# Optimization experiments

Hardware: AMD Instinct MI355X
Metric: run time of the kernel (lower is better)

## Reference

```python
import jax, jax.numpy as jnp
import numpy as np

NUM_SEQ, NUM_RES = 512, 768
MSA_C, PAIR_C, NUM_HEAD = 64, 128, 8
VALUE_DIM = MSA_C // NUM_HEAD
EPS = 1e-5


def _layernorm(x, scale, bias):
    mu = jnp.mean(x, axis=-1, keepdims=True)
    var = jnp.var(x, axis=-1, keepdims=True)
    return (x - mu) * jax.lax.rsqrt(var + EPS) * scale + bias


def setup_inputs() -> dict:
    key = jax.random.key(0)
    ks = jax.random.split(key, 8)
    act = jax.random.normal(ks[0], (NUM_SEQ, NUM_RES, MSA_C), dtype=jnp.float32)
    mask = jnp.ones((NUM_SEQ, NUM_RES), dtype=jnp.float32)
    pair_act = jax.random.normal(ks[1], (NUM_RES, NUM_RES, PAIR_C), dtype=jnp.float32)
    # learned params
    act_scale = jnp.ones((MSA_C,), jnp.float32)
    act_bias = jnp.zeros((MSA_C,), jnp.float32)
    pair_scale = jnp.ones((PAIR_C,), jnp.float32)
    pair_bias = jnp.zeros((PAIR_C,), jnp.float32)
    w_pair_logits = jax.random.normal(ks[2], (NUM_HEAD, PAIR_C), jnp.float32) * (PAIR_C ** -0.5)
    v_proj = jax.random.normal(ks[3], (MSA_C, NUM_HEAD, VALUE_DIM), jnp.float32) * (MSA_C ** -0.5)
    w_gate = jax.random.normal(ks[4], (MSA_C, MSA_C), jnp.float32) * (MSA_C ** -0.5)
    w_out = jax.random.normal(ks[5], (MSA_C, MSA_C), jnp.float32) * (MSA_C ** -0.5)
    return {
        "act": act, "mask": mask, "pair_act": pair_act,
        "act_scale": act_scale, "act_bias": act_bias,
        "pair_scale": pair_scale, "pair_bias": pair_bias,
        "w_pair_logits": w_pair_logits, "v_proj": v_proj,
        "w_gate": w_gate, "w_out": w_out,
    }


def reference(act, mask, pair_act, act_scale, act_bias, pair_scale, pair_bias,
              w_pair_logits, v_proj, w_gate, w_out):
    act = _layernorm(act, act_scale, act_bias)            # [b, k, i]
    pair = _layernorm(pair_act, pair_scale, pair_bias)    # [q, k, c]
    logits = jnp.einsum('qkc,hc->hqk', pair, w_pair_logits)  # [h, q, k]
    # mask reduced over MSA rows; torch casts to bf16 before the bias add
    mask_max = jnp.max(mask, axis=0).astype(jnp.bfloat16)    # [k]
    logits = logits + 1e9 * (mask_max.astype(logits.dtype) - 1.0)
    weights = jax.nn.softmax(logits, axis=-1)                # [h, q, k]
    v = jnp.einsum('bki,ihc->bkhc', act, v_proj)             # [b, k, h, c]
    v_avg = jnp.einsum('hqk,bkhc->bqhc', weights, v)         # [b, q, h, c]
    v_avg = v_avg.reshape(v_avg.shape[0], v_avg.shape[1], -1)  # [b, q, h*c]
    gate = jax.nn.sigmoid(act @ w_gate.T)
    return (v_avg * gate) @ w_out.T
```

## Files before the change

kernel.cpp:

```cpp
#include <hip/hip_runtime.h>
#include <hip/hip_bf16.h>

#define NSEQ 512
#define NRES 768
#define MSAC 64
#define PAIRC 128
#define NHEAD 8

typedef __attribute__((ext_vector_type(8))) short short8_t;
typedef __attribute__((ext_vector_type(4))) float f32x4;

__device__ __forceinline__ float bf2f(unsigned short u){
  return __uint_as_float(((unsigned int)u) << 16);
}
__device__ __forceinline__ unsigned short f2bf(float f){
  unsigned int x = __float_as_uint(f);
  x += 0x7fffu + ((x >> 16) & 1u);
  return (unsigned short)(x >> 16);
}
__device__ __forceinline__ void glds16(const void* g, void* l){
  __builtin_amdgcn_global_load_lds(
      (const __attribute__((address_space(1))) unsigned int*)g,
      (__attribute__((address_space(3))) unsigned int*)l, 16, 0, 0);
}

__global__ __launch_bounds__(256) void k_prep2(
    const float* __restrict__ mask, const float* __restrict__ vproj,
    const float* __restrict__ wgate, const float* __restrict__ wout,
    const float* __restrict__ pscale, const float* __restrict__ pbias,
    const float* __restrict__ wl,
    float* __restrict__ bias, unsigned short* __restrict__ WvT,
    unsigned short* __restrict__ WgT, unsigned short* __restrict__ WoH,
    unsigned short* __restrict__ WoL, unsigned short* __restrict__ WST,
    float* __restrict__ AB)
{
  const int bid = blockIdx.x, tid = threadIdx.x;
  if (bid < 12){
    __shared__ float red[4][64];
    const int kk = bid*64 + (tid & 63);
    const int bs = tid >> 6;
    float m = -1e30f;
    for (int b = bs; b < NSEQ; b += 4) m = fmaxf(m, mask[(size_t)b*NRES + kk]);
    red[bs][tid & 63] = m;
    __syncthreads();
    if (tid < 64){
      float mm = fmaxf(fmaxf(red[0][tid], red[1][tid]),
                       fmaxf(red[2][tid], red[3][tid]));
      bias[bid*64 + tid] = 1e9f * (bf2f(f2bf(mm)) - 1.0f);
    }
  } else if (bid < 28){
    const int t = (bid - 12)*256 + tid;
    const int j = t >> 6, i = t & 63;
    WvT[t] = f2bf(vproj[i*64 + j]);
    WgT[t] = f2bf(wgate[t]);
    float wv = wout[t];
    unsigned short hh = f2bf(wv);
    WoH[t] = hh;
    WoL[t] = f2bf(wv - bf2f(hh));
  } else {
    #pragma unroll
    for (int i = 0; i < 4; ++i){
      int t = i*256 + tid;
      int h = t >> 7, c = t & 127;
      float w = pscale[c] * wl[h*PAIRC + c];
      unsigned short hh = f2bf(w);
      WST[h*PAIRC + c] = hh;
      WST[(h + 8)*PAIRC + c] = f2bf(w - bf2f(hh));
    }
    const int h = tid >> 5, cc = tid & 31;
    float pa = 0.f, pb = 0.f;
    for (int c = cc; c < PAIRC; c += 32){
      float w = wl[h*PAIRC + c];
      pa += pscale[c]*w;  pb += pbias[c]*w;
    }
    #pragma unroll
    for (int m = 1; m < 32; m <<= 1){
      pa += __shfl_xor(pa, m, 64);
      pb += __shfl_xor(pb, m, 64);
    }
    if (cc == 0){ AB[h] = pa; AB[8 + h] = pb; }
  }
}

__global__ __launch_bounds__(256) void k_pair(
    const float* __restrict__ pair, const unsigned short* __restrict__ WST,
    const float* __restrict__ AB, const float* __restrict__ mbias,
    unsigned short* __restrict__ weights)
{
  __shared__ float lg[NHEAD][NRES];
  const int q = blockIdx.x;
  const int tid = threadIdx.x;
  const int wv = tid >> 6, lane = tid & 63;
  const int lr = lane & 15, lcq = lane >> 4;

  short8_t wfrag[4];
  #pragma unroll
  for (int s = 0; s < 4; ++s)
    wfrag[s] = *(const short8_t*)(WST + lr*PAIRC + lcq*8 + s*32);

  const int hb = (lcq & 1) * 4;
  float A4[4], B4[4];
  #pragma unroll
  for (int r = 0; r < 4; ++r){ A4[r] = AB[hb + r]; B4[r] = AB[8 + hb + r]; }

  for (int tile = wv; tile < 48; tile += 4){
    const int k0 = tile * 16;
    const float* base = pair + ((size_t)q*NRES + k0 + lr)*PAIRC + lcq*8;
    f32x4 a1 = 0.f, a2 = 0.f;
    float s = 0.f, ss = 0.f;
    #pragma unroll
    for (int st = 0; st < 4; ++st){
      float4 u0 = *(const float4*)(base + st*32);
      float4 u1 = *(const float4*)(base + st*32 + 4);
      float xv[8] = {u0.x,u0.y,u0.z,u0.w,u1.x,u1.y,u1.z,u1.w};
      short8_t xh, xl;
      #pragma unroll
      for (int e = 0; e < 8; ++e){
        s += xv[e]; ss += xv[e]*xv[e];
        unsigned short hi = f2bf(xv[e]);
        xh[e] = (short)hi;
        xl[e] = (short)f2bf(xv[e] - bf2f(hi));
      }
      a1 = __builtin_amdgcn_mfma_f32_16x16x32_bf16(wfrag[st], xh, a1, 0, 0, 0);
      a2 = __builtin_amdgcn_mfma_f32_16x16x32_bf16(wfrag[st], xl, a2, 0, 0, 0);
    }
    s  += __shfl_xor(s, 16, 64);  ss += __shfl_xor(ss, 16, 64);
    s  += __shfl_xor(s, 32, 64);  ss += __shfl_xor(ss, 32, 64);
    const float mu  = s * (1.f/128.f);
    const float var = ss * (1.f/128.f) - mu*mu;
    const float rsq = rsqrtf(var + 1e-5f);
    float d[4];
    #pragma unroll
    for (int r = 0; r < 4; ++r)
      d[r] = a1[r] + __shfl_xor(a1[r], 32, 64) + a2[r];
    if (lane < 32){
      const int k = k0 + lr;
      #pragma unroll
      for (int r = 0; r < 4; ++r)
        lg[hb + r][k] = rsq * (d[r] - mu * A4[r]) + B4[r];
    }
  }
  __syncthreads();
  #pragma unroll
  for (int hh = 0; hh < 2; ++hh){
    int h = wv + hh*4;
    float mx = -1e30f;
    for (int kk = lane; kk < NRES; kk += 64) mx = fmaxf(mx, lg[h][kk] + mbias[kk]);
    #pragma unroll
    for (int m = 1; m < 64; m <<= 1) mx = fmaxf(mx, __shfl_xor(mx, m, 64));
    float sum = 0.f;
    for (int kk = lane; kk < NRES; kk += 64){
      float e = __expf(lg[h][kk] + mbias[kk] - mx);
      lg[h][kk] = e; sum += e;
    }
    #pragma unroll
    for (int m = 1; m < 64; m <<= 1) sum += __shfl_xor(sum, m, 64);
    float inv = 1.0f / sum;
    unsigned short* wrow = weights + ((size_t)h * NRES + q) * NRES;
    for (int kk = lane; kk < NRES; kk += 64) wrow[kk] = f2bf(lg[h][kk] * inv);
  }
}

__global__ __launch_bounds__(512) void k_act(
    const float* __restrict__ act, const float* __restrict__ ascale,
    const float* __restrict__ abias, const unsigned short* __restrict__ WvT,
    const unsigned short* __restrict__ WgT, unsigned short* __restrict__ v,
    unsigned short* __restrict__ gate)
{
  __shared__ __align__(16) unsigned char sm[18432];
  unsigned short (*vt)[72] = (unsigned short (*)[72])sm;
  unsigned short (*gt)[72] = (unsigned short (*)[72])(sm + 9216);
  const int abid = blockIdx.x;
  const int b  = abid / 6;
  const int k0 = (abid % 6) * 128;
  const int tid = threadIdx.x;
  const int w = tid >> 6, lane = tid & 63;
  const int lr = lane & 15;
  const int lc = lane >> 4;
  const int row = k0 + w*16 + lr;

  short8_t bv[4][2], bg[4][2];
  #pragma unroll
  for (int mf = 0; mf < 4; ++mf){
    #pragma unroll
    for (int s = 0; s < 2; ++s){
      bv[mf][s] = *(const short8_t*)(WvT + (mf*16 + lr)*64 + s*32 + lc*8);
      bg[mf][s] = *(const short8_t*)(WgT + (mf*16 + lr)*64 + s*32 + lc*8);
    }
  }

  const float* arow = act + ((size_t)b*NRES + row)*MSAC;
  float x[2][8];
  #pragma unroll
  for (int s = 0; s < 2; ++s){
    float4 t0 = *(const float4*)(arow + s*32 + lc*8);
    float4 t1 = *(const float4*)(arow + s*32 + lc*8 + 4);
    x[s][0]=t0.x; x[s][1]=t0.y; x[s][2]=t0.z; x[s][3]=t0.w;
    x[s][4]=t1.x; x[s][5]=t1.y; x[s][6]=t1.z; x[s][7]=t1.w;
  }
  float ps = 0.f, pss = 0.f;
  #pragma unroll
  for (int s = 0; s < 2; ++s)
    #pragma unroll
    for (int e = 0; e < 8; ++e){ ps += x[s][e]; pss += x[s][e]*x[s][e]; }
  ps  += __shfl_xor(ps, 16, 64);  pss += __shfl_xor(pss, 16, 64);
  ps  += __shfl_xor(ps, 32, 64);  pss += __shfl_xor(pss, 32, 64);
  const float mu  = ps * (1.f/64.f);
  const float var = pss * (1.f/64.f) - mu*mu;
  const float rs  = rsqrtf(var + 1e-5f);

  short8_t a[2];
  #pragma unroll
  for (int s = 0; s < 2; ++s){
    float4 s0 = *(const float4*)(ascale + s*32 + lc*8);
    float4 s1 = *(const float4*)(ascale + s*32 + lc*8 + 4);
    float4 b0 = *(const float4*)(abias  + s*32 + lc*8);
    float4 b1 = *(const float4*)(abias  + s*32 + lc*8 + 4);
    const float sc[8] = {s0.x,s0.y,s0.z,s0.w,s1.x,s1.y,s1.z,s1.w};
    const float bs[8] = {b0.x,b0.y,b0.z,b0.w,b1.x,b1.y,b1.z,b1.w};
    #pragma unroll
    for (int e = 0; e < 8; ++e)
      a[s][e] = (short)f2bf((x[s][e] - mu)*rs*sc[e] + bs[e]);
  }

  f32x4 accv[4], accg[4];
  #pragma unroll
  for (int mf = 0; mf < 4; ++mf){ accv[mf] = 0.f; accg[mf] = 0.f; }
  #pragma unroll
  for (int mf = 0; mf < 4; ++mf){
    #pragma unroll
    for (int s = 0; s < 2; ++s){
      accv[mf] = __builtin_amdgcn_mfma_f32_16x16x32_bf16(a[s], bv[mf][s], accv[mf], 0, 0, 0);
      accg[mf] = __builtin_amdgcn_mfma_f32_16x16x32_bf16(bg[mf][s], a[s], accg[mf], 0, 0, 0);
    }
  }

  #pragma unroll
  for (int pass = 0; pass < 2; ++pass){
    if ((w >> 2) == pass){
      const int wl2 = w & 3;
      #pragma unroll
      for (int mf = 0; mf < 4; ++mf){
        ushort4 ov;
        ov.x = f2bf(accv[mf][0]); ov.y = f2bf(accv[mf][1]);
        ov.z = f2bf(accv[mf][2]); ov.w = f2bf(accv[mf][3]);
        *(ushort4*)&vt[mf*16 + lr][wl2*16 + lc*4] = ov;
        ushort4 og;
        og.x = f2bf(1.0f/(1.0f + __expf(-accg[mf][0])));
        og.y = f2bf(1.0f/(1.0f + __expf(-accg[mf][1])));
        og.z = f2bf(1.0f/(1.0f + __expf(-accg[mf][2])));
        og.w = f2bf(1.0f/(1.0f + __expf(-accg[mf][3])));
        *(ushort4*)&gt[wl2*16 + lr][mf*16 + lc*4] = og;
      }
    }
    __syncthreads();
    {
      const int kbase = k0 + pass*64;
      const int j = tid >> 3, chunk = tid & 7;
      uint4 val = *(const uint4*)&vt[j][chunk*8];
      *(uint4*)(v + ((size_t)(j >> 3)*4096 + (size_t)b*8 + (j & 7))*NRES + kbase + chunk*8) = val;
      uint4 gval = *(const uint4*)&gt[j][chunk*8];
      *(uint4*)(gate + ((size_t)b*NRES + kbase + j)*MSAC + chunk*8) = gval;
    }
    __syncthreads();
  }
}

__global__ __launch_bounds__(256) void k_wavg(
    const unsigned short* __restrict__ V, const unsigned short* __restrict__ W,
    unsigned short* __restrict__ Y)
{
  __shared__ unsigned char smem[32768];

  const int flat = blockIdx.x;
  const int nid  = (flat & 7) * 192 + (flat >> 3);
  const int m    = nid % 192;
  const int by   = m % 6;
  const int bx   = m / 6;
  const int h    = nid / 192;

  const int tid = threadIdx.x, wid = tid >> 6, lane = tid & 63;
  const int wm = wid & 1, wn = wid >> 1;
  const unsigned short* Ag = V + (size_t)h*4096*768 + (size_t)bx*128*768;
  const unsigned short* Bg = W + (size_t)h*768*768 + (size_t)by*128*768;

  f32x4 acc[4][4];
  #pragma unroll
  for (int i=0;i<4;++i){
    #pragma unroll
    for (int jj=0;jj<4;++jj) acc[i][jj] = 0.f;
  }

  #define STAGE_K(bufsel, kt) { \
    unsigned char* Ab = smem + (bufsel)*16384; \
    unsigned char* Bb = Ab + 8192; \
    _Pragma("unroll") \
    for (int r = 0; r < 2; ++r){ \
      int cid = tid + r*256; \
      int rw = cid >> 2, ch = cid & 3; \
      int sc = ch ^ ((rw >> 1) & 3); \
      glds16(Ag + (size_t)rw*768 + (kt)*32 + sc*8, Ab + cid*16 - lane*16); \
      glds16(Bg + (size_t)rw*768 + (kt)*32 + sc*8, Bb + cid*16 - lane*16); \
    } }

  STAGE_K(0, 0);
  __syncthreads();
  const int c0 = lane >> 4;
  for (int kt = 0; kt < 24; ++kt){
    if (kt < 23) STAGE_K((kt+1)&1, kt+1);
    unsigned char* Ab = smem + (kt&1)*16384;
    unsigned char* Bb = Ab + 8192;
    short8_t af[4], bf[4];
    #pragma unroll
    for (int mf = 0; mf < 4; ++mf){
      int row = wm*64 + mf*16 + (lane & 15);
      int off = row*64 + ((c0 ^ ((row>>1)&3)) << 4);
      af[mf] = *(const short8_t*)(Ab + off);
    }
    #pragma unroll
    for (int nf = 0; nf < 4; ++nf){
      int row = wn*64 + nf*16 + (lane & 15);
      int off = row*64 + ((c0 ^ ((row>>1)&3)) << 4);
      bf[nf] = *(const short8_t*)(Bb + off);
    }
    #pragma unroll
    for (int mf = 0; mf < 4; ++mf){
      #pragma unroll
      for (int nf = 0; nf < 4; ++nf)
        acc[mf][nf] = __builtin_amdgcn_mfma_f32_16x16x32_bf16(af[mf], bf[nf], acc[mf][nf], 0, 0, 0);
    }
    __syncthreads();
  }
  #undef STAGE_K

  unsigned char* Ds = smem;
  #pragma unroll
  for (int mf = 0; mf < 4; ++mf){
    int bc = wm*64 + mf*16 + ((lane >> 4) << 2);
    #pragma unroll
    for (int nf = 0; nf < 4; ++nf){
      int q = wn*64 + nf*16 + (lane & 15);
      f32x4 a = acc[mf][nf];
      ushort4 o;
      o.x = f2bf(a[0]); o.y = f2bf(a[1]); o.z = f2bf(a[2]); o.w = f2bf(a[3]);
      int off = q*256 + bc*2; off ^= (q & 7) << 4;
      *(ushort4*)(Ds + off) = o;
    }
  }
  __syncthreads();
  unsigned short* Yb = Y + ((size_t)(h*32 + bx)*768 + by*128)*128;
  #pragma unroll
  for (int it = 0; it < 8; ++it){
    int fl = it*256 + tid;
    int q = fl >> 4, chunk = fl & 15;
    int off = q*256 + chunk*16; off ^= (q & 7) << 4;
    uint4 val = *(const uint4*)(Ds + off);
    *(uint4*)(Yb + (size_t)fl*8) = val;
  }
}

__global__ __launch_bounds__(256) void k_final(
    const unsigned short* __restrict__ Y, const unsigned short* __restrict__ gate,
    const unsigned short* __restrict__ WoH, const unsigned short* __restrict__ WoL,
    float* __restrict__ out)
{
  const int p = blockIdx.x;
  const int r = p & 7, t = p >> 3;
  const int b  = r*64 + (t & 63);
  const int q0 = (t >> 6) * 64;
  const int tid = threadIdx.x, w = tid >> 6, lane = tid & 63;
  const int lr = lane & 15, lc = lane >> 4;

  short8_t bh[4][2], bl[4][2];
  #pragma unroll
  for (int nf = 0; nf < 4; ++nf){
    #pragma unroll
    for (int s = 0; s < 2; ++s){
      bh[nf][s] = *(const short8_t*)(WoH + (nf*16 + lr)*64 + s*32 + lc*8);
      bl[nf][s] = *(const short8_t*)(WoL + (nf*16 + lr)*64 + s*32 + lc*8);
    }
  }

  const int q = q0 + w*16 + lr;
  short8_t ah[2], al[2];
  #pragma unroll
  for (int s = 0; s < 2; ++s){
    const int hh = s*4 + lc;
    short8_t y8 = *(const short8_t*)(Y + ((size_t)(hh*32 + (b >> 4))*768 + q)*128 + (b & 15)*8);
    short8_t g8 = *(const short8_t*)(gate + ((size_t)b*NRES + q)*MSAC + s*32 + lc*8);
    #pragma unroll
    for (int e = 0; e < 8; ++e){
      float pp = bf2f((unsigned short)y8[e]) * bf2f((unsigned short)g8[e]);
      unsigned short hi = f2bf(pp);
      ah[s][e] = (short)hi;
      al[s][e] = (short)f2bf(pp - bf2f(hi));
    }
  }

  f32x4 acc[4];
  #pragma unroll
  for (int nf = 0; nf < 4; ++nf) acc[nf] = 0.f;
  #pragma unroll
  for (int nf = 0; nf < 4; ++nf){
    #pragma unroll
    for (int s = 0; s < 2; ++s){
      acc[nf] = __builtin_amdgcn_mfma_f32_16x16x32_bf16(ah[s], bh[nf][s], acc[nf], 0, 0, 0);
      acc[nf] = __builtin_amdgcn_mfma_f32_16x16x32_bf16(al[s], bh[nf][s], acc[nf], 0, 0, 0);
      acc[nf] = __builtin_amdgcn_mfma_f32_16x16x32_bf16(ah[s], bl[nf][s], acc[nf], 0, 0, 0);
    }
  }

  #pragma unroll
  for (int nf = 0; nf < 4; ++nf){
    #pragma unroll
    for (int e = 0; e < 4; ++e){
      int qq = q0 + w*16 + lc*4 + e;
      out[((size_t)b*NRES + qq)*MSAC + nf*16 + lr] = acc[nf][e];
    }
  }
}

extern "C" void kernel_launch(void* const* d_in, const int* in_sizes, int n_in,
                              void* d_out, int out_size, void* d_ws, size_t ws_size,
                              hipStream_t stream) {
  (void)in_sizes; (void)n_in; (void)out_size; (void)ws_size;
  const float* act    = (const float*)d_in[0];
  const float* mask   = (const float*)d_in[1];
  const float* pair   = (const float*)d_in[2];
  const float* ascale = (const float*)d_in[3];
  const float* abias  = (const float*)d_in[4];
  const float* pscale = (const float*)d_in[5];
  const float* pbias  = (const float*)d_in[6];
  const float* wl     = (const float*)d_in[7];
  const float* vproj  = (const float*)d_in[8];
  const float* wgate  = (const float*)d_in[9];
  const float* wout   = (const float*)d_in[10];
  float* out = (float*)d_out;

  char* ws = (char*)d_ws;
  float*          mbias   = (float*)(ws);
  unsigned short* WvT     = (unsigned short*)(ws + 4096);
  unsigned short* WgT     = (unsigned short*)(ws + 12288);
  unsigned short* WoH     = (unsigned short*)(ws + 20480);
  unsigned short* WoL     = (unsigned short*)(ws + 28672);
  unsigned short* WST     = (unsigned short*)(ws + 36864);
  float*          AB      = (float*)(ws + 40960);
  unsigned short* weights = (unsigned short*)(ws + 45056);
  unsigned short* v       = (unsigned short*)(ws + 45056 + 9437184);
  unsigned short* gate    = (unsigned short*)(ws + 45056 + 9437184 + 50331648);
  unsigned short* y       = (unsigned short*)(ws + 45056 + 9437184 + 2*50331648ull);

  k_prep2<<<dim3(29), dim3(256), 0, stream>>>(mask, vproj, wgate, wout,
                                              pscale, pbias, wl,
                                              mbias, WvT, WgT, WoH, WoL, WST, AB);
  k_pair<<<dim3(768), dim3(256), 0, stream>>>(pair, WST, AB, mbias, weights);
  k_act<<<dim3(3072), dim3(512), 0, stream>>>(act, ascale, abias, WvT, WgT, v, gate);
  k_wavg<<<dim3(1536), dim3(256), 0, stream>>>(v, weights, y);
  k_final<<<dim3(6144), dim3(256), 0, stream>>>(y, gate, WoH, WoL, out);
}
```

Before: 309.1 us.

## Double-buffer pair tiles via async LDS loads and split softmax into separate kernel

The pair-logit kernel now stages each wave's 16-row pair tiles into swizzled LDS with global_load_lds and double buffers them, so the next tile's loads overlap the MFMA and layernorm work on the current one. Softmax moves out into a new k_soft kernel that reads fp32 logits from a global scratch buffer, which frees the pair kernel's shared-memory logits array. The cost is an extra launch and a roughly 19 MB fp32 logits round trip through memory. The pair kernel's 64KB of LDS per block also limits how many blocks fit on a CU.

```diff
diff --git a/kernel.cpp b/kernel.cpp
--- a/kernel.cpp
+++ b/kernel.cpp
@@ -84,10 +84,9 @@
 
 __global__ __launch_bounds__(256) void k_pair(
     const float* __restrict__ pair, const unsigned short* __restrict__ WST,
-    const float* __restrict__ AB, const float* __restrict__ mbias,
-    unsigned short* __restrict__ weights)
+    const float* __restrict__ AB, float* __restrict__ logits)
 {
-  __shared__ float lg[NHEAD][NRES];
+  __shared__ __align__(16) unsigned char sm[65536];
   const int q = blockIdx.x;
   const int tid = threadIdx.x;
   const int wv = tid >> 6, lane = tid & 63;
@@ -103,15 +102,35 @@
   #pragma unroll
   for (int r = 0; r < 4; ++r){ A4[r] = AB[hb + r]; B4[r] = AB[8 + hb + r]; }
 
-  for (int tile = wv; tile < 48; tile += 4){
-    const int k0 = tile * 16;
-    const float* base = pair + ((size_t)q*NRES + k0 + lr)*PAIRC + lcq*8;
+  unsigned char* wbuf = sm + wv*16384;
+
+#define STAGEP(bufp, tile_) { \
+    const float* gsrc_ = pair + ((size_t)q*NRES + (tile_)*16)*PAIRC; \
+    _Pragma("unroll") \
+    for (int j = 0; j < 8; ++j){ \
+      int rowj_ = 2*j + (lane >> 5); \
+      int cd_ = lane & 31; \
+      int sc_ = cd_ ^ (rowj_ & 7); \
+      glds16(gsrc_ + (size_t)rowj_*PAIRC + sc_*4, (bufp) + j*1024); \
+    } }
+
+  STAGEP(wbuf,        wv);
+  STAGEP(wbuf + 8192, wv + 4);
+
+  for (int i = 0; i < 12; ++i){
+    const int tile = wv + 4*i;
+    if (i < 11) asm volatile("s_waitcnt vmcnt(8)" ::: "memory");
+    else        asm volatile("s_waitcnt vmcnt(0)" ::: "memory");
+    __builtin_amdgcn_sched_barrier(0);
+    unsigned char* cb = wbuf + (i & 1)*8192;
+
     f32x4 a1 = 0.f, a2 = 0.f;
     float s = 0.f, ss = 0.f;
     #pragma unroll
     for (int st = 0; st < 4; ++st){
-      float4 u0 = *(const float4*)(base + st*32);
-      float4 u1 = *(const float4*)(base + st*32 + 4);
+      const int c16 = lcq*2 + st*8;
+      float4 u0 = *(const float4*)(cb + lr*512 + ((c16     ^ (lr & 7)) << 4));
+      float4 u1 = *(const float4*)(cb + lr*512 + (((c16+1) ^ (lr & 7)) << 4));
       float xv[8] = {u0.x,u0.y,u0.z,u0.w,u1.x,u1.y,u1.z,u1.w};
       short8_t xh, xl;
       #pragma unroll
@@ -134,30 +153,51 @@
     for (int r = 0; r < 4; ++r)
       d[r] = a1[r] + __shfl_xor(a1[r], 32, 64) + a2[r];
     if (lane < 32){
-      const int k = k0 + lr;
+      const int k = tile*16 + lr;
       #pragma unroll
       for (int r = 0; r < 4; ++r)
-        lg[hb + r][k] = rsq * (d[r] - mu * A4[r]) + B4[r];
-    }
+        logits[(size_t)q*6144 + (hb + r)*768 + k] = rsq * (d[r] - mu * A4[r]) + B4[r];
+    }
+
+    if (i + 2 < 12){
+      __builtin_amdgcn_sched_barrier(0);
+      STAGEP(cb, wv + 4*(i + 2));
+    }
+  }
+#undef STAGEP
+}
+
+__global__ __launch_bounds__(256) void k_soft(
+    const float* __restrict__ logits, const float* __restrict__ mbias,
+    unsigned short* __restrict__ weights)
+{
+  __shared__ float lgf[6144];
+  const int q = blockIdx.x, tid = threadIdx.x;
+  const float* src = logits + (size_t)q*6144;
+  #pragma unroll
+  for (int i = 0; i < 6; ++i){
+    int idx = (i*256 + tid)*4;
+    *(float4*)&lgf[idx] = *(const float4*)(src + idx);
   }
   __syncthreads();
+  const int wv = tid >> 6, lane = tid & 63;
   #pragma unroll
   for (int hh = 0; hh < 2; ++hh){
     int h = wv + hh*4;
     float mx = -1e30f;
-    for (int kk = lane; kk < NRES; kk += 64) mx = fmaxf(mx, lg[h][kk] + mbias[kk]);
+    for (int kk = lane; kk < NRES; kk += 64) mx = fmaxf(mx, lgf[h*768 + kk] + mbias[kk]);
     #pragma unroll
     for (int m = 1; m < 64; m <<= 1) mx = fmaxf(mx, __shfl_xor(mx, m, 64));
     float sum = 0.f;
     for (int kk = lane; kk < NRES; kk += 64){
-      float e = __expf(lg[h][kk] + mbias[kk] - mx);
-      lg[h][kk] = e; sum += e;
+      float e = __expf(lgf[h*768 + kk] + mbias[kk] - mx);
+      lgf[h*768 + kk] = e; sum += e;
     }
     #pragma unroll
     for (int m = 1; m < 64; m <<= 1) sum += __shfl_xor(sum, m, 64);
     float inv = 1.0f / sum;
     unsigned short* wrow = weights + ((size_t)h * NRES + q) * NRES;
-    for (int kk = lane; kk < NRES; kk += 64) wrow[kk] = f2bf(lg[h][kk] * inv);
+    for (int kk = lane; kk < NRES; kk += 64) wrow[kk] = f2bf(lgf[h*768 + kk] * inv);
   }
 }
 
@@ -449,11 +489,13 @@
   unsigned short* v       = (unsigned short*)(ws + 45056 + 9437184);
   unsigned short* gate    = (unsigned short*)(ws + 45056 + 9437184 + 50331648);
   unsigned short* y       = (unsigned short*)(ws + 45056 + 9437184 + 2*50331648ull);
+  float*          logits  = (float*)(ws + 45056 + 9437184 + 3*50331648ull);
 
   k_prep2<<<dim3(29), dim3(256), 0, stream>>>(mask, vproj, wgate, wout,
                                               pscale, pbias, wl,
                                               mbias, WvT, WgT, WoH, WoL, WST, AB);
-  k_pair<<<dim3(768), dim3(256), 0, stream>>>(pair, WST, AB, mbias, weights);
+  k_pair<<<dim3(768), dim3(256), 0, stream>>>(pair, WST, AB, logits);
+  k_soft<<<dim3(768), dim3(256), 0, stream>>>(logits, mbias, weights);
   k_act<<<dim3(3072), dim3(512), 0, stream>>>(act, ascale, abias, WvT, WgT, v, gate);
   k_wavg<<<dim3(1536), dim3(256), 0, stream>>>(v, weights, y);
   k_final<<<dim3(6144), dim3(256), 0, stream>>>(y, gate, WoH, WoL, out);
```

New measurement: 325.3 us. 1.05x slower.

## Split pair-logit kernel into quarter-row blocks and a separate softmax kernel

Applied to the files above, without the earlier changes.

The pair layernorm+logit projection kernel now launches four blocks per query row, each covering a quarter of the key tiles, and writes fp32 logits to a global workspace. A new softmax kernel reloads each row's logits into shared memory, applies the mask bias and softmax, and writes bf16 weights. The aim is more parallelism and occupancy on the bandwidth-heavy pair read, since the old 768-block grid was small for the GPU. In exchange it adds an extra launch and a write and re-read of a 18.9 MB logit buffer.

```diff
diff --git a/kernel.cpp b/kernel.cpp
--- a/kernel.cpp
+++ b/kernel.cpp
@@ -84,11 +84,10 @@
 
 __global__ __launch_bounds__(256) void k_pair(
     const float* __restrict__ pair, const unsigned short* __restrict__ WST,
-    const float* __restrict__ AB, const float* __restrict__ mbias,
-    unsigned short* __restrict__ weights)
-{
-  __shared__ float lg[NHEAD][NRES];
-  const int q = blockIdx.x;
+    const float* __restrict__ AB, float* __restrict__ logits)
+{
+  const int q = blockIdx.x >> 2;
+  const int quarter = blockIdx.x & 3;
   const int tid = threadIdx.x;
   const int wv = tid >> 6, lane = tid & 63;
   const int lr = lane & 15, lcq = lane >> 4;
@@ -103,7 +102,9 @@
   #pragma unroll
   for (int r = 0; r < 4; ++r){ A4[r] = AB[hb + r]; B4[r] = AB[8 + hb + r]; }
 
-  for (int tile = wv; tile < 48; tile += 4){
+  #pragma unroll
+  for (int i = 0; i < 3; ++i){
+    const int tile = quarter*12 + wv + 4*i;
     const int k0 = tile * 16;
     const float* base = pair + ((size_t)q*NRES + k0 + lr)*PAIRC + lcq*8;
     f32x4 a1 = 0.f, a2 = 0.f;
@@ -137,27 +138,42 @@
       const int k = k0 + lr;
       #pragma unroll
       for (int r = 0; r < 4; ++r)
-        lg[hb + r][k] = rsq * (d[r] - mu * A4[r]) + B4[r];
-    }
+        logits[(size_t)q*6144 + (hb + r)*768 + k] = rsq * (d[r] - mu * A4[r]) + B4[r];
+    }
+  }
+}
+
+__global__ __launch_bounds__(256) void k_soft(
+    const float* __restrict__ logits, const float* __restrict__ mbias,
+    unsigned short* __restrict__ weights)
+{
+  __shared__ float lgf[6144];
+  const int q = blockIdx.x, tid = threadIdx.x;
+  const float* src = logits + (size_t)q*6144;
+  #pragma unroll
+  for (int i = 0; i < 6; ++i){
+    int idx = (i*256 + tid)*4;
+    *(float4*)&lgf[idx] = *(const float4*)(src + idx);
   }
   __syncthreads();
+  const int wv = tid >> 6, lane = tid & 63;
   #pragma unroll
   for (int hh = 0; hh < 2; ++hh){
     int h = wv + hh*4;
     float mx = -1e30f;
-    for (int kk = lane; kk < NRES; kk += 64) mx = fmaxf(mx, lg[h][kk] + mbias[kk]);
+    for (int kk = lane; kk < NRES; kk += 64) mx = fmaxf(mx, lgf[h*768 + kk] + mbias[kk]);
     #pragma unroll
     for (int m = 1; m < 64; m <<= 1) mx = fmaxf(mx, __shfl_xor(mx, m, 64));
     float sum = 0.f;
     for (int kk = lane; kk < NRES; kk += 64){
-      float e = __expf(lg[h][kk] + mbias[kk] - mx);
-      lg[h][kk] = e; sum += e;
+      float e = __expf(lgf[h*768 + kk] + mbias[kk] - mx);
+      lgf[h*768 + kk] = e; sum += e;
     }
     #pragma unroll
     for (int m = 1; m < 64; m <<= 1) sum += __shfl_xor(sum, m, 64);
     float inv = 1.0f / sum;
     unsigned short* wrow = weights + ((size_t)h * NRES + q) * NRES;
-    for (int kk = lane; kk < NRES; kk += 64) wrow[kk] = f2bf(lg[h][kk] * inv);
+    for (int kk = lane; kk < NRES; kk += 64) wrow[kk] = f2bf(lgf[h*768 + kk] * inv);
   }
 }
 
@@ -449,11 +465,13 @@
   unsigned short* v       = (unsigned short*)(ws + 45056 + 9437184);
   unsigned short* gate    = (unsigned short*)(ws + 45056 + 9437184 + 50331648);
   unsigned short* y       = (unsigned short*)(ws + 45056 + 9437184 + 2*50331648ull);
+  float*          logits  = (float*)(ws + 45056 + 9437184 + 3*50331648ull);
 
   k_prep2<<<dim3(29), dim3(256), 0, stream>>>(mask, vproj, wgate, wout,
                                               pscale, pbias, wl,
                                               mbias, WvT, WgT, WoH, WoL, WST, AB);
-  k_pair<<<dim3(768), dim3(256), 0, stream>>>(pair, WST, AB, mbias, weights);
+  k_pair<<<dim3(3072), dim3(256), 0, stream>>>(pair, WST, AB, logits);
+  k_soft<<<dim3(768), dim3(256), 0, stream>>>(logits, mbias, weights);
   k_act<<<dim3(3072), dim3(512), 0, stream>>>(act, ascale, abias, WvT, WgT, v, gate);
   k_wavg<<<dim3(1536), dim3(256), 0, stream>>>(v, weights, y);
   k_final<<<dim3(6144), dim3(256), 0, stream>>>(y, gate, WoH, WoL, out);
```

Result: slower. 317.5 us (+2.7%).
